# Performance work log

Measured on AMD Instinct MI355X. Metric: run time of the kernel, lower is better.

## Reference

```python
import jax, jax.numpy as jnp
import numpy as np

T = 0.2          # temperature
W = 0.1          # loss weight
BIG = 2 ** 30    # sentinel label for masked-out samples


def setup_inputs() -> dict:
    key = jax.random.key(0)
    k1, k2, k3, k4 = jax.random.split(key, 4)
    bs, C, Gn, S = 32, 128, 256, 16
    grouped_features = jax.random.normal(k1, (bs, C, Gn, S), dtype=jnp.float32)
    # instance labels in [-1, 8): -1 = background
    proposal_instance_mask = jax.random.randint(k2, (bs, Gn, S), -1, 8, dtype=jnp.int32)
    # seed indices with duplicates possible (range 40 over 16 samples)
    grouped_indices = jax.random.randint(k3, (bs, Gn, S), 0, 40, dtype=jnp.int32)
    context_compen = jax.random.normal(k4, (1, C), dtype=jnp.float32)
    return {
        "proposal_instance_mask": proposal_instance_mask,
        "grouped_features": grouped_features,
        "grouped_indices": grouped_indices,
        "context_compen": context_compen,
    }


def _group_loss(feat, idx, lab, ctx):
    # feat: [S, C], idx: [S], lab: [S], ctx: [C]
    # NOTE: sum_{a,b} f_a . g_b / (n_f * n_g) == mean(f) . mean(g), so the
    # original tiny-mm contrastive loss reduces to pairwise dots of per-instance means.
    S, C = feat.shape
    pos = jnp.arange(S)
    # unique count of seed indices -> truncate to first u samples (as in torch code)
    si = jnp.sort(idx)
    u = 1 + jnp.sum(si[1:] != si[:-1])
    valid = pos < u
    lab_m = jnp.where(valid, lab, BIG)
    # per-group unique labels (sorted), jit-friendly
    sl = jnp.sort(lab_m)
    new = jnp.concatenate([jnp.ones((1,), bool), sl[1:] != sl[:-1]])
    cid = jnp.cumsum(new) - 1                      # compact id of each sorted label
    uniq = jnp.full((S,), BIG, sl.dtype).at[cid].set(sl)
    n_labels = jnp.sum(new & (sl != BIG))          # number of distinct valid labels
    has_bg = uniq[0] == -1                         # -1 sorts first if present
    # per-instance mean features via segment scatter-add
    comp = jnp.searchsorted(uniq, lab_m)           # sample -> compact instance slot
    sums = jnp.zeros((S, C), feat.dtype).at[comp].add(jnp.where(valid[:, None], feat, 0.0))
    cnts = jnp.zeros((S,), feat.dtype).at[comp].add(valid.astype(feat.dtype))
    means = sums / jnp.maximum(cnts, 1.0)[:, None]
    hb = has_bg.astype(jnp.int32)
    fg_count = n_labels - hb
    inst_num = fg_count + 1                        # bg slot always present
    # row 0 = bg mean (or context_compen if no bg), rows 1.. = fg means
    gidx = jnp.clip(pos + hb - 1, 0, S - 1)
    M = means[gidx]
    M = M.at[0].set(jnp.where(has_bg, M[0], ctx))
    inst_valid = pos < inst_num
    sim = (M @ M.T) / T                            # [S, S] tiny matmul of means
    sim_m = jnp.where(inst_valid[None, :], sim, -jnp.inf)
    lse = jax.scipy.special.logsumexp(sim_m, axis=1)
    li = lse - jnp.diagonal(sim)                   # -log(pos/(pos+neg)) per fg row
    fg_mask = inst_valid & (pos >= 1)
    gl = jnp.sum(jnp.where(fg_mask, li, 0.0)) / jnp.maximum(inst_num - 1, 1).astype(feat.dtype)
    return gl, fg_count >= 1


def reference(proposal_instance_mask, grouped_features, grouped_indices, context_compen):
    bs, C, Gn, S = grouped_features.shape
    feats = grouped_features.transpose(0, 2, 3, 1).reshape(-1, S, C)  # [G, S, C]
    idxs = grouped_indices.reshape(-1, S)
    labs = proposal_instance_mask.reshape(-1, S)
    ctx = context_compen[0]
    gl, gv = jax.vmap(lambda f, i, l: _group_loss(f, i, l, ctx))(feats, idxs, labs)
    gvf = gv.astype(gl.dtype)
    return jnp.sum(gl * gvf) / jnp.sum(gvf) * W
```

## Files before the change

kernel.cpp:

```cpp
#include <hip/hip_runtime.h>

#define GQ   8192
#define WPB  2
#define MROW 132
#define SLICE 1280

__global__ __launch_bounds__(64 * WPB, 6) void group_loss_kernel(
    const int*   __restrict__ labs,
    const float* __restrict__ feats,
    const int*   __restrict__ idxs,
    const float* __restrict__ ctx,
    float2* __restrict__ ws)
{
    __shared__ float SH[WPB * SLICE];

    const int l  = threadIdx.x & 63;
    const int wu = threadIdx.x >> 6;
    float* MM   = SH + wu * SLICE;
    float* SIMM = MM + 9 * MROW;

    const int blk = blockIdx.x;
    const int g  = ((blk & 7) << 10) | ((blk >> 3) << 1) | wu;
    const int b  = g >> 8;
    const int gn = g & 255;
    const long fbase = (long)b * (128 * 256 * 16) + (long)gn * 16;

    const float* gp0 = feats + fbase + (long)l * 4096;
    const float* gp1 = gp0 + 64 * 4096;
    float4 A[4], B[4];
    #pragma unroll
    for (int q = 0; q < 4; ++q) A[q] = *(const float4*)(gp0 + q * 4);
    #pragma unroll
    for (int q = 0; q < 4; ++q) B[q] = *(const float4*)(gp1 + q * 4);
    const float cx0 = ctx[l], cx1 = ctx[l + 64];
    float fa[16], fb[16];
    #pragma unroll
    for (int q = 0; q < 4; ++q) {
        fa[4*q+0] = A[q].x; fa[4*q+1] = A[q].y; fa[4*q+2] = A[q].z; fa[4*q+3] = A[q].w;
        fb[4*q+0] = B[q].x; fb[4*q+1] = B[q].y; fb[4*q+2] = B[q].z; fb[4*q+3] = B[q].w;
    }

    int myidx = -1, mylab = -2;
    if (l < 16) { myidx = idxs[g * 16 + l]; mylab = labs[g * 16 + l]; }

    bool dup = false;
    #pragma unroll
    for (int j = 0; j < 15; ++j) {
        const int vj = __shfl(myidx, j);
        dup = dup || ((l > j) && (myidx == vj));
    }
    const int u = __popcll(__ballot((l < 16) && !dup));

    const bool valid = l < u;
    const int bid = valid ? (mylab + 1) : 255;

    unsigned long long memb[9]; int cnt[9];
    #pragma unroll
    for (int r = 0; r < 9; ++r) {
        memb[r] = __ballot(bid == r);
        cnt[r]  = __popcll(memb[r]);
    }
    const bool has_bg = cnt[0] > 0;
    int fg_count = 0, pm = 0;
    #pragma unroll
    for (int r = 1; r < 9; ++r)
        if (cnt[r] > 0) { ++fg_count; pm |= 1 << r; }

    float m0[9] = {0,0,0,0,0,0,0,0,0};
    float m1[9] = {0,0,0,0,0,0,0,0,0};
    #pragma unroll
    for (int s = 0; s < 16; ++s) {
        if (s < u) {
            const int bs = __builtin_amdgcn_readlane(bid, s);
            switch (bs) {
                case 0: m0[0] += fa[s]; m1[0] += fb[s]; break;
                case 1: m0[1] += fa[s]; m1[1] += fb[s]; break;
                case 2: m0[2] += fa[s]; m1[2] += fb[s]; break;
                case 3: m0[3] += fa[s]; m1[3] += fb[s]; break;
                case 4: m0[4] += fa[s]; m1[4] += fb[s]; break;
                case 5: m0[5] += fa[s]; m1[5] += fb[s]; break;
                case 6: m0[6] += fa[s]; m1[6] += fb[s]; break;
                case 7: m0[7] += fa[s]; m1[7] += fb[s]; break;
                case 8: m0[8] += fa[s]; m1[8] += fb[s]; break;
            }
        }
    }
    #pragma unroll
    for (int r = 0; r < 9; ++r) {
        const float invc = 1.0f / (float)(cnt[r] > 0 ? cnt[r] : 1);
        m0[r] *= invc; m1[r] *= invc;
    }
    if (!has_bg) { m0[0] = cx0; m1[0] = cx1; }

    #pragma unroll
    for (int r = 0; r < 9; ++r) {
        MM[r * MROW + l]      = m0[r];
        MM[r * MROW + 64 + l] = m1[r];
    }
    __syncthreads();

    float simv = 0.0f; int pi = 0, pj = 0;
    if (l < 44) {
        pi = (int)((sqrtf(8.0f * (float)l + 9.0f) - 1.0f) * 0.5f);
        pj = l - (pi * (pi + 1) / 2 - 1);
        const float* Ri = MM + pi * MROW;
        const float* Rj = MM + pj * MROW;
        float acc = 0.0f;
        #pragma unroll
        for (int q = 0; q < 32; ++q) {
            float4 x = *(const float4*)(Ri + 4 * q);
            float4 y = *(const float4*)(Rj + 4 * q);
            acc += x.x * y.x + x.y * y.y + x.z * y.z + x.w * y.w;
        }
        simv = acc * 5.0f;
    }
    if (l < 44) {
        SIMM[pi * 9 + pj] = simv;
        if (pi != pj) SIMM[pj * 9 + pi] = simv;
    }
    __syncthreads();

    float li_val = 0.0f;
    if (l >= 1 && l < 9 && ((pm >> l) & 1)) {
        float srow[9];
        #pragma unroll
        for (int j = 0; j < 9; ++j) srow[j] = SIMM[l * 9 + j];
        float vmax = srow[0];
        #pragma unroll
        for (int j = 1; j < 9; ++j)
            if ((pm >> j) & 1) vmax = fmaxf(vmax, srow[j]);
        float se = __expf(srow[0] - vmax);
        #pragma unroll
        for (int j = 1; j < 9; ++j)
            if ((pm >> j) & 1) se += __expf(srow[j] - vmax);
        li_val = vmax + __logf(se) - srow[l];
    }

    float ssum = li_val;
    #pragma unroll
    for (int off = 8; off >= 1; off >>= 1) ssum += __shfl_down(ssum, off);
    if (l == 0) {
        float2 r;
        r.x = ssum / (float)(fg_count > 0 ? fg_count : 1);
        r.y = (fg_count > 0) ? 1.0f : 0.0f;
        ws[g] = r;
    }
}

__global__ __launch_bounds__(1024) void reduce_kernel(
    const float2* __restrict__ ws, float* __restrict__ out)
{
    __shared__ float sa[1024], sb[1024];
    const int t = threadIdx.x;
    float a = 0.0f, b2 = 0.0f;
    for (int g = t; g < GQ; g += 1024) {
        float2 v = ws[g];
        a += v.x; b2 += v.y;
    }
    sa[t] = a; sb[t] = b2;
    __syncthreads();
    for (int off = 512; off > 0; off >>= 1) {
        if (t < off) { sa[t] += sa[t + off]; sb[t] += sb[t + off]; }
        __syncthreads();
    }
    if (t == 0) out[0] = 0.1f * (sa[0] / sb[0]);
}

extern "C" void kernel_launch(void* const* d_in, const int* in_sizes, int n_in,
                              void* d_out, int out_size, void* d_ws, size_t ws_size,
                              hipStream_t stream) {
    const int*   labs  = (const int*)d_in[0];
    const float* feats = (const float*)d_in[1];
    const int*   idxs  = (const int*)d_in[2];
    const float* ctx   = (const float*)d_in[3];
    float* out = (float*)d_out;
    float2* ws = (float2*)d_ws;

    group_loss_kernel<<<GQ / WPB, 64 * WPB, 0, stream>>>(labs, feats, idxs, ctx, ws);
    reduce_kernel<<<1, 1024, 0, stream>>>(ws, out);
}
```

Before: 112.0 us.

## Process two groups per wavefront with wider loads and LDS-only fences

Each wavefront now handles two adjacent groups, so every lane loads 32 contiguous floats per channel (two groups' samples) and 32 lanes fetch indices and labels at once. Block-wide __syncthreads are replaced with s_waitcnt lgkmcnt(0) fences, because each wave only touches its own LDS slice. The dot product is split across four independent accumulators to shorten the dependency chain. The launch-bounds occupancy hint drops from 6 to 4 to make room for the extra registers. This halves the block count and adds more memory-level parallelism per wave, at the cost of more register pressure and reliance on wave-local LDS ordering.

```diff
diff --git a/kernel.cpp b/kernel.cpp
--- a/kernel.cpp
+++ b/kernel.cpp
@@ -2,10 +2,14 @@
 
 #define GQ   8192
 #define WPB  2
+#define GPW  2
 #define MROW 132
 #define SLICE 1280
 
-__global__ __launch_bounds__(64 * WPB, 6) void group_loss_kernel(
+#define LDS_FENCE() asm volatile("s_waitcnt lgkmcnt(0)" ::: "memory")
+#define COMP(v4, k) ((k)==0?(v4).x:((k)==1?(v4).y:((k)==2?(v4).z:(v4).w)))
+
+__global__ __launch_bounds__(64 * WPB, 4) void group_loss_kernel(
     const int*   __restrict__ labs,
     const float* __restrict__ feats,
     const int*   __restrict__ idxs,
@@ -20,130 +24,134 @@
     float* SIMM = MM + 9 * MROW;
 
     const int blk = blockIdx.x;
-    const int g  = ((blk & 7) << 10) | ((blk >> 3) << 1) | wu;
-    const int b  = g >> 8;
-    const int gn = g & 255;
+    const int gbase = ((blk & 7) << 10) | ((blk >> 3) << 2) | (wu << 1);
+    const int b  = gbase >> 8;
+    const int gn = gbase & 255;
     const long fbase = (long)b * (128 * 256 * 16) + (long)gn * 16;
 
-    const float* gp0 = feats + fbase + (long)l * 4096;
-    const float* gp1 = gp0 + 64 * 4096;
-    float4 A[4], B[4];
-    #pragma unroll
-    for (int q = 0; q < 4; ++q) A[q] = *(const float4*)(gp0 + q * 4);
-    #pragma unroll
-    for (int q = 0; q < 4; ++q) B[q] = *(const float4*)(gp1 + q * 4);
-    const float cx0 = ctx[l], cx1 = ctx[l + 64];
-    float fa[16], fb[16];
+    const float* gp = feats + fbase + (long)l * 4096;
+    float4 A[2][4], B[2][4];
     #pragma unroll
     for (int q = 0; q < 4; ++q) {
-        fa[4*q+0] = A[q].x; fa[4*q+1] = A[q].y; fa[4*q+2] = A[q].z; fa[4*q+3] = A[q].w;
-        fb[4*q+0] = B[q].x; fb[4*q+1] = B[q].y; fb[4*q+2] = B[q].z; fb[4*q+3] = B[q].w;
+        A[0][q] = *(const float4*)(gp + q * 4);
+        A[1][q] = *(const float4*)(gp + 16 + q * 4);
+        B[0][q] = *(const float4*)(gp + 64 * 4096 + q * 4);
+        B[1][q] = *(const float4*)(gp + 64 * 4096 + 16 + q * 4);
     }
+    int raw_idx = 0, raw_lab = -2;
+    if (l < 32) { raw_idx = idxs[gbase * 16 + l]; raw_lab = labs[gbase * 16 + l]; }
+    const float cx0 = ctx[l], cx1 = ctx[l + 64];
 
-    int myidx = -1, mylab = -2;
-    if (l < 16) { myidx = idxs[g * 16 + l]; mylab = labs[g * 16 + l]; }
+    #pragma unroll
+    for (int t = 0; t < GPW; ++t) {
+        const int g = gbase + t;
 
-    bool dup = false;
-    #pragma unroll
-    for (int j = 0; j < 15; ++j) {
-        const int vj = __shfl(myidx, j);
-        dup = dup || ((l > j) && (myidx == vj));
-    }
-    const int u = __popcll(__ballot((l < 16) && !dup));
+        const int myidx = __shfl(raw_idx, (l & 15) + 16 * t);
+        const int mylab = __shfl(raw_lab, (l & 15) + 16 * t);
 
-    const bool valid = l < u;
-    const int bid = valid ? (mylab + 1) : 255;
+        bool dup = false;
+        #pragma unroll
+        for (int j = 0; j < 15; ++j) {
+            const int vj = __shfl(myidx, j);
+            dup = dup || ((l > j) && (myidx == vj));
+        }
+        const int u = __popcll(__ballot((l < 16) && !dup));
 
-    unsigned long long memb[9]; int cnt[9];
-    #pragma unroll
-    for (int r = 0; r < 9; ++r) {
-        memb[r] = __ballot(bid == r);
-        cnt[r]  = __popcll(memb[r]);
-    }
-    const bool has_bg = cnt[0] > 0;
-    int fg_count = 0, pm = 0;
-    #pragma unroll
-    for (int r = 1; r < 9; ++r)
-        if (cnt[r] > 0) { ++fg_count; pm |= 1 << r; }
+        const bool valid = l < u;
+        const int bid = valid ? (mylab + 1) : 255;
 
-    float m0[9] = {0,0,0,0,0,0,0,0,0};
-    float m1[9] = {0,0,0,0,0,0,0,0,0};
-    #pragma unroll
-    for (int s = 0; s < 16; ++s) {
-        if (s < u) {
-            const int bs = __builtin_amdgcn_readlane(bid, s);
-            switch (bs) {
-                case 0: m0[0] += fa[s]; m1[0] += fb[s]; break;
-                case 1: m0[1] += fa[s]; m1[1] += fb[s]; break;
-                case 2: m0[2] += fa[s]; m1[2] += fb[s]; break;
-                case 3: m0[3] += fa[s]; m1[3] += fb[s]; break;
-                case 4: m0[4] += fa[s]; m1[4] += fb[s]; break;
-                case 5: m0[5] += fa[s]; m1[5] += fb[s]; break;
-                case 6: m0[6] += fa[s]; m1[6] += fb[s]; break;
-                case 7: m0[7] += fa[s]; m1[7] += fb[s]; break;
-                case 8: m0[8] += fa[s]; m1[8] += fb[s]; break;
+        int cnt[9];
+        #pragma unroll
+        for (int r = 0; r < 9; ++r) cnt[r] = __popcll(__ballot(bid == r));
+        const bool has_bg = cnt[0] > 0;
+        int fg_count = 0, pm = 0;
+        #pragma unroll
+        for (int r = 1; r < 9; ++r)
+            if (cnt[r] > 0) { ++fg_count; pm |= 1 << r; }
+
+        float m0[9] = {0,0,0,0,0,0,0,0,0};
+        float m1[9] = {0,0,0,0,0,0,0,0,0};
+        #pragma unroll
+        for (int s = 0; s < 16; ++s) {
+            if (s < u) {
+                const int bs = __builtin_amdgcn_readlane(bid, s);
+                const float fas = COMP(A[t][s >> 2], s & 3);
+                const float fbs = COMP(B[t][s >> 2], s & 3);
+                switch (bs) {
+                    case 0: m0[0] += fas; m1[0] += fbs; break;
+                    case 1: m0[1] += fas; m1[1] += fbs; break;
+                    case 2: m0[2] += fas; m1[2] += fbs; break;
+                    case 3: m0[3] += fas; m1[3] += fbs; break;
+                    case 4: m0[4] += fas; m1[4] += fbs; break;
+                    case 5: m0[5] += fas; m1[5] += fbs; break;
+                    case 6: m0[6] += fas; m1[6] += fbs; break;
+                    case 7: m0[7] += fas; m1[7] += fbs; break;
+                    case 8: m0[8] += fas; m1[8] += fbs; break;
+                }
             }
         }
-    }
-    #pragma unroll
-    for (int r = 0; r < 9; ++r) {
-        const float invc = 1.0f / (float)(cnt[r] > 0 ? cnt[r] : 1);
-        m0[r] *= invc; m1[r] *= invc;
-    }
-    if (!has_bg) { m0[0] = cx0; m1[0] = cx1; }
+        #pragma unroll
+        for (int r = 0; r < 9; ++r) {
+            const float invc = 1.0f / (float)(cnt[r] > 0 ? cnt[r] : 1);
+            m0[r] *= invc; m1[r] *= invc;
+        }
+        if (!has_bg) { m0[0] = cx0; m1[0] = cx1; }
 
-    #pragma unroll
-    for (int r = 0; r < 9; ++r) {
-        MM[r * MROW + l]      = m0[r];
-        MM[r * MROW + 64 + l] = m1[r];
-    }
-    __syncthreads();
+        LDS_FENCE();
+        #pragma unroll
+        for (int r = 0; r < 9; ++r) {
+            MM[r * MROW + l]      = m0[r];
+            MM[r * MROW + 64 + l] = m1[r];
+        }
+        LDS_FENCE();
 
-    float simv = 0.0f; int pi = 0, pj = 0;
-    if (l < 44) {
-        pi = (int)((sqrtf(8.0f * (float)l + 9.0f) - 1.0f) * 0.5f);
-        pj = l - (pi * (pi + 1) / 2 - 1);
-        const float* Ri = MM + pi * MROW;
-        const float* Rj = MM + pj * MROW;
-        float acc = 0.0f;
+        float simv = 0.0f; int pi = 0, pj = 0;
+        if (l < 44) {
+            pi = (int)((sqrtf(8.0f * (float)l + 9.0f) - 1.0f) * 0.5f);
+            pj = l - (pi * (pi + 1) / 2 - 1);
+            const float* Ri = MM + pi * MROW;
+            const float* Rj = MM + pj * MROW;
+            float ax = 0.f, ay = 0.f, az = 0.f, aw = 0.f;
+            #pragma unroll
+            for (int q = 0; q < 32; ++q) {
+                float4 x = *(const float4*)(Ri + 4 * q);
+                float4 y = *(const float4*)(Rj + 4 * q);
+                ax += x.x * y.x; ay += x.y * y.y;
+                az += x.z * y.z; aw += x.w * y.w;
+            }
+            simv = ((ax + ay) + (az + aw)) * 5.0f;
+        }
+        if (l < 44) {
+            SIMM[pi * 9 + pj] = simv;
+            if (pi != pj) SIMM[pj * 9 + pi] = simv;
+        }
+        LDS_FENCE();
+
+        float li_val = 0.0f;
+        if (l >= 1 && l < 9 && ((pm >> l) & 1)) {
+            float srow[9];
+            #pragma unroll
+            for (int j = 0; j < 9; ++j) srow[j] = SIMM[l * 9 + j];
+            float vmax = srow[0];
+            #pragma unroll
+            for (int j = 1; j < 9; ++j)
+                if ((pm >> j) & 1) vmax = fmaxf(vmax, srow[j]);
+            float se = __expf(srow[0] - vmax);
+            #pragma unroll
+            for (int j = 1; j < 9; ++j)
+                if ((pm >> j) & 1) se += __expf(srow[j] - vmax);
+            li_val = vmax + __logf(se) - srow[l];
+        }
+
+        float ssum = li_val;
         #pragma unroll
-        for (int q = 0; q < 32; ++q) {
-            float4 x = *(const float4*)(Ri + 4 * q);
-            float4 y = *(const float4*)(Rj + 4 * q);
-            acc += x.x * y.x + x.y * y.y + x.z * y.z + x.w * y.w;
+        for (int off = 8; off >= 1; off >>= 1) ssum += __shfl_down(ssum, off);
+        if (l == 0) {
+            float2 r;
+            r.x = ssum / (float)(fg_count > 0 ? fg_count : 1);
+            r.y = (fg_count > 0) ? 1.0f : 0.0f;
+            ws[g] = r;
         }
-        simv = acc * 5.0f;
-    }
-    if (l < 44) {
-        SIMM[pi * 9 + pj] = simv;
-        if (pi != pj) SIMM[pj * 9 + pi] = simv;
-    }
-    __syncthreads();
-
-    float li_val = 0.0f;
-    if (l >= 1 && l < 9 && ((pm >> l) & 1)) {
-        float srow[9];
-        #pragma unroll
-        for (int j = 0; j < 9; ++j) srow[j] = SIMM[l * 9 + j];
-        float vmax = srow[0];
-        #pragma unroll
-        for (int j = 1; j < 9; ++j)
-            if ((pm >> j) & 1) vmax = fmaxf(vmax, srow[j]);
-        float se = __expf(srow[0] - vmax);
-        #pragma unroll
-        for (int j = 1; j < 9; ++j)
-            if ((pm >> j) & 1) se += __expf(srow[j] - vmax);
-        li_val = vmax + __logf(se) - srow[l];
-    }
-
-    float ssum = li_val;
-    #pragma unroll
-    for (int off = 8; off >= 1; off >>= 1) ssum += __shfl_down(ssum, off);
-    if (l == 0) {
-        float2 r;
-        r.x = ssum / (float)(fg_count > 0 ? fg_count : 1);
-        r.y = (fg_count > 0) ? 1.0f : 0.0f;
-        ws[g] = r;
     }
 }
 
@@ -176,6 +184,6 @@
     float* out = (float*)d_out;
     float2* ws = (float2*)d_ws;
 
-    group_loss_kernel<<<GQ / WPB, 64 * WPB, 0, stream>>>(labs, feats, idxs, ctx, ws);
+    group_loss_kernel<<<GQ / (WPB * GPW), 64 * WPB, 0, stream>>>(labs, feats, idxs, ctx, ws);
     reduce_kernel<<<1, 1024, 0, stream>>>(ws, out);
 }
```

New measurement: 115.2 us. +2.8%, slower.

## Compute Gram entries with DPP wave reductions instead of LDS staging and barriers

Applied to the files above, without the earlier changes.

Drops the per-wave shared-memory staging of the 9x128 instance-mean matrix and the two block barriers. Each of the 44 lower-triangle similarity entries is now computed by a DPP wave-wide sum and read back with readlane, and only the packed triangle goes through LDS, fenced by an s_waitcnt instead of __syncthreads. The duplicate-index scan uses readlane plus ballot instead of shuffles, and the final row sum uses DPP. In exchange each wave runs 44 serial reduction chains of roughly six DPP adds each, and the launch-bounds occupancy hint drops from 6 to 4.

```diff
diff --git a/kernel.cpp b/kernel.cpp
--- a/kernel.cpp
+++ b/kernel.cpp
@@ -2,22 +2,46 @@
 
 #define GQ   8192
 #define WPB  2
-#define MROW 132
-#define SLICE 1280
 
-__global__ __launch_bounds__(64 * WPB, 6) void group_loss_kernel(
+#define LDS_FENCE() asm volatile("s_waitcnt lgkmcnt(0)" ::: "memory")
+
+template <int CTRL>
+__device__ __forceinline__ float dpp_add(float x) {
+    int t = __builtin_amdgcn_update_dpp(0, __float_as_int(x), CTRL, 0xf, 0xf, true);
+    return x + __int_as_float(t);
+}
+__device__ __forceinline__ float wave_sum64(float x) {
+    x = dpp_add<0x111>(x);
+    x = dpp_add<0x112>(x);
+    x = dpp_add<0x114>(x);
+    x = dpp_add<0x118>(x);
+    x = dpp_add<0x142>(x);
+    x = dpp_add<0x143>(x);
+    return x;
+}
+__device__ __forceinline__ float row_sum16(float x) {
+    x = dpp_add<0x111>(x);
+    x = dpp_add<0x112>(x);
+    x = dpp_add<0x114>(x);
+    x = dpp_add<0x118>(x);
+    return x;
+}
+__device__ __forceinline__ float rdlane_f(float x, int lane) {
+    return __int_as_float(__builtin_amdgcn_readlane(__float_as_int(x), lane));
+}
+
+__global__ __launch_bounds__(64 * WPB, 4) void group_loss_kernel(
     const int*   __restrict__ labs,
     const float* __restrict__ feats,
     const int*   __restrict__ idxs,
     const float* __restrict__ ctx,
     float2* __restrict__ ws)
 {
-    __shared__ float SH[WPB * SLICE];
+    __shared__ float SH[WPB * 48];
 
     const int l  = threadIdx.x & 63;
     const int wu = threadIdx.x >> 6;
-    float* MM   = SH + wu * SLICE;
-    float* SIMM = MM + 9 * MROW;
+    float* SIMM = SH + wu * 48;
 
     const int blk = blockIdx.x;
     const int g  = ((blk & 7) << 10) | ((blk >> 3) << 1) | wu;
@@ -43,23 +67,21 @@
     int myidx = -1, mylab = -2;
     if (l < 16) { myidx = idxs[g * 16 + l]; mylab = labs[g * 16 + l]; }
 
-    bool dup = false;
+    unsigned long long dupm = 0ULL;
     #pragma unroll
     for (int j = 0; j < 15; ++j) {
-        const int vj = __shfl(myidx, j);
-        dup = dup || ((l > j) && (myidx == vj));
+        const int sj = __builtin_amdgcn_readlane(myidx, j);
+        const unsigned long long eq = __ballot(myidx == sj);
+        dupm |= (eq & ~((2ULL << j) - 1ULL));
     }
-    const int u = __popcll(__ballot((l < 16) && !dup));
+    const int u = __popcll(~dupm & 0xFFFFULL);
 
     const bool valid = l < u;
     const int bid = valid ? (mylab + 1) : 255;
 
-    unsigned long long memb[9]; int cnt[9];
+    int cnt[9];
     #pragma unroll
-    for (int r = 0; r < 9; ++r) {
-        memb[r] = __ballot(bid == r);
-        cnt[r]  = __popcll(memb[r]);
-    }
+    for (int r = 0; r < 9; ++r) cnt[r] = __popcll(__ballot(bid == r));
     const bool has_bg = cnt[0] > 0;
     int fg_count = 0, pm = 0;
     #pragma unroll
@@ -92,39 +114,36 @@
     }
     if (!has_bg) { m0[0] = cx0; m1[0] = cx1; }
 
-    #pragma unroll
-    for (int r = 0; r < 9; ++r) {
-        MM[r * MROW + l]      = m0[r];
-        MM[r * MROW + 64 + l] = m1[r];
+    float mine = 0.0f;
+    {
+        int p = 0;
+        #pragma unroll
+        for (int i = 1; i <= 8; ++i) {
+            #pragma unroll
+            for (int j = 0; j <= i; ++j) {
+                float x = m0[i] * m0[j] + m1[i] * m1[j];
+                x = wave_sum64(x);
+                const float sv = rdlane_f(x, 63);
+                mine = (l == p) ? sv : mine;
+                ++p;
+            }
+        }
     }
-    __syncthreads();
+    mine *= 5.0f;
 
-    float simv = 0.0f; int pi = 0, pj = 0;
-    if (l < 44) {
-        pi = (int)((sqrtf(8.0f * (float)l + 9.0f) - 1.0f) * 0.5f);
-        pj = l - (pi * (pi + 1) / 2 - 1);
-        const float* Ri = MM + pi * MROW;
-        const float* Rj = MM + pj * MROW;
-        float acc = 0.0f;
-        #pragma unroll
-        for (int q = 0; q < 32; ++q) {
-            float4 x = *(const float4*)(Ri + 4 * q);
-            float4 y = *(const float4*)(Rj + 4 * q);
-            acc += x.x * y.x + x.y * y.y + x.z * y.z + x.w * y.w;
-        }
-        simv = acc * 5.0f;
-    }
-    if (l < 44) {
-        SIMM[pi * 9 + pj] = simv;
-        if (pi != pj) SIMM[pj * 9 + pi] = simv;
-    }
-    __syncthreads();
+    if (l < 44) SIMM[l] = mine;
+    LDS_FENCE();
 
     float li_val = 0.0f;
     if (l >= 1 && l < 9 && ((pm >> l) & 1)) {
+        const int r = l;
         float srow[9];
         #pragma unroll
-        for (int j = 0; j < 9; ++j) srow[j] = SIMM[l * 9 + j];
+        for (int j = 0; j < 9; ++j) {
+            const int ii = (r > j) ? r : j;
+            const int jj = (r > j) ? j : r;
+            srow[j] = SIMM[ii * (ii + 1) / 2 - 1 + jj];
+        }
         float vmax = srow[0];
         #pragma unroll
         for (int j = 1; j < 9; ++j)
@@ -133,15 +152,14 @@
         #pragma unroll
         for (int j = 1; j < 9; ++j)
             if ((pm >> j) & 1) se += __expf(srow[j] - vmax);
-        li_val = vmax + __logf(se) - srow[l];
+        li_val = vmax + __logf(se) - srow[r];
     }
 
-    float ssum = li_val;
-    #pragma unroll
-    for (int off = 8; off >= 1; off >>= 1) ssum += __shfl_down(ssum, off);
+    const float ssum = row_sum16(li_val);
+    const float tot  = rdlane_f(ssum, 15);
     if (l == 0) {
         float2 r;
-        r.x = ssum / (float)(fg_count > 0 ? fg_count : 1);
+        r.x = tot / (float)(fg_count > 0 ? fg_count : 1);
         r.y = (fg_count > 0) ? 1.0f : 0.0f;
         ws[g] = r;
     }
```

After: 115.2 us. 1.03x slower.
